# Optimization experiments

Hardware: AMD Instinct MI355X
Metric: run time of the kernel (lower is better)

The kernel has to match this reference:

```python
import jax, jax.numpy as jnp
import numpy as np

N = 100000
E = 1600000
IN_C = 128
OUT_C = 64
HID = 2 * OUT_C  # 128


def setup_inputs() -> dict:
    key = jax.random.key(0)
    ks = jax.random.split(key, 10)
    s = lambda fan_in: 1.0 / np.sqrt(fan_in)
    inp = {
        "x": jax.random.normal(ks[0], (N, IN_C), dtype=jnp.float32),
        "edge_index": jax.random.randint(ks[1], (2, E), 0, N, dtype=jnp.int64),
        # SAGEConv params: lin_l acts on aggregated neighbors (with bias), lin_r on root (no bias)
        "W1l": jax.random.uniform(ks[2], (IN_C, HID), jnp.float32, -s(IN_C), s(IN_C)),
        "b1": jnp.zeros((HID,), jnp.float32),
        "W1r": jax.random.uniform(ks[3], (IN_C, HID), jnp.float32, -s(IN_C), s(IN_C)),
        "Wml": jax.random.uniform(ks[4], (HID, OUT_C), jnp.float32, -s(HID), s(HID)),
        "bm": jnp.zeros((OUT_C,), jnp.float32),
        "Wmr": jax.random.uniform(ks[5], (HID, OUT_C), jnp.float32, -s(HID), s(HID)),
        "Wsl": jax.random.uniform(ks[6], (HID, OUT_C), jnp.float32, -s(HID), s(HID)),
        "bs": jnp.zeros((OUT_C,), jnp.float32),
        "Wsr": jax.random.uniform(ks[7], (HID, OUT_C), jnp.float32, -s(HID), s(HID)),
    }
    return inp


def _sage_mean(x, src, dst, Wl, b, Wr):
    n = x.shape[0]
    # mean aggregation of source features onto destination nodes
    agg = jax.ops.segment_sum(x[src], dst, num_segments=n)
    cnt = jax.ops.segment_sum(jnp.ones((src.shape[0],), x.dtype), dst, num_segments=n)
    agg = agg / jnp.maximum(cnt, 1.0)[:, None]
    return agg @ Wl + b + x @ Wr


def reference(x, edge_index, W1l, b1, W1r, Wml, bm, Wmr, Wsl, bs, Wsr):
    src, dst = edge_index[0], edge_index[1]
    h = jax.nn.relu(_sage_mean(x, src, dst, W1l, b1, W1r))
    mu = _sage_mean(h, src, dst, Wml, bm, Wmr)
    logstd = _sage_mean(h, src, dst, Wsl, bs, Wsr)
    return mu, logstd
```

## Files before the change

### kernel.cpp

```cpp
#include <hip/hip_runtime.h>


typedef __attribute__((ext_vector_type(8))) short bf16x8;
typedef __attribute__((ext_vector_type(4))) float f32x4;
typedef __attribute__((ext_vector_type(2))) float f32x2;

#define SHIFT 9
#define BW 512

__device__ __forceinline__ unsigned short f2bf(float f) {
    unsigned u = __builtin_bit_cast(unsigned, f);
    u += 0x7fff + ((u >> 16) & 1);
    return (unsigned short)(u >> 16);
}
__device__ __forceinline__ float bflo(unsigned u) { return __builtin_bit_cast(float, u << 16); }
__device__ __forceinline__ float bfh(unsigned u) { return __builtin_bit_cast(float, u); }

__global__ __launch_bounds__(256) void stage1_kernel(
    const float* __restrict__ x, const int* __restrict__ raw,
    const float* __restrict__ W1l, const float* __restrict__ W1r,
    const float* __restrict__ Wml, const float* __restrict__ Wmr,
    const float* __restrict__ Wsl, const float* __restrict__ Wsr,
    const float* __restrict__ bm, const float* __restrict__ bs,
    unsigned short* __restrict__ B1p, unsigned short* __restrict__ B2p,
    float* __restrict__ bc, unsigned short* __restrict__ A1,
    unsigned short* __restrict__ A2, int* __restrict__ bcnt,
    unsigned* __restrict__ recs, int n, int nE, int cap, int nBinA, int nXB) {
    const int b = blockIdx.x;
    const int t = threadIdx.x;
    if (b < nBinA) {
        __shared__ int cnt[256];
        __shared__ int cur[256];
        __shared__ int gbase[256];
        __shared__ int sflag;
        const int e0 = b * 4096;
        const int e1 = (e0 + 4096 < nE) ? e0 + 4096 : nE;
        int acc = 0;
        for (int e = e0 + t; e < e1; e += 256) acc |= raw[2 * e + 1];
        if (t == 0) sflag = 0;
        cnt[t] = 0;
        cur[t] = 0;
        __syncthreads();
        if (acc) atomicOr(&sflag, 1);
        __syncthreads();
        const bool is64 = (sflag == 0);
        for (int e = e0 + t; e < e1; e += 256) {
            int d = is64 ? raw[2 * (nE + e)] : raw[nE + e];
            atomicAdd(&cnt[d >> SHIFT], 1);
        }
        __syncthreads();
        gbase[t] = cnt[t] ? atomicAdd(&bcnt[t], cnt[t]) : 0;
        __syncthreads();
        for (int e = e0 + t; e < e1; e += 256) {
            int s, d;
            if (is64) { s = raw[2 * e]; d = raw[2 * (nE + e)]; }
            else      { s = raw[e];     d = raw[nE + e]; }
            int bk = d >> SHIFT;
            int pos = gbase[bk] + atomicAdd(&cur[bk], 1);
            if (pos < cap)
                recs[(size_t)bk * cap + pos] = ((unsigned)s << SHIFT) | (unsigned)(d & (BW - 1));
        }
    } else if (b < nBinA + nXB) {
        int i = ((b - nBinA) * 256 + t) * 4;
        if (i < n * 128) {
            float4 v = *reinterpret_cast<const float4*>(x + i);
            int row = i >> 7, col = i & 127;
            unsigned short* p = A1 + (size_t)row * 256 + 128 + col;
            p[0] = f2bf(v.x); p[1] = f2bf(v.y); p[2] = f2bf(v.z); p[3] = f2bf(v.w);
        }
    } else if (b < nBinA + nXB + 128) {
        int i = (b - nBinA - nXB) * 256 + t;
        int j = i & 7, lq = (i >> 3) & 63, ks = (i >> 9) & 7, nf = i >> 12;
        int k = ks * 32 + (lq >> 4) * 8 + j;
        int c = nf * 16 + (lq & 15);
        float w1 = (k < 128) ? W1l[k * 128 + c] : W1r[(k - 128) * 128 + c];
        float w2;
        if (k < 128) w2 = (c < 64) ? Wml[k * 64 + c] : Wsl[k * 64 + (c - 64)];
        else         w2 = (c < 64) ? Wmr[(k - 128) * 64 + c] : Wsr[(k - 128) * 64 + (c - 64)];
        B1p[i] = f2bf(w1);
        B2p[i] = f2bf(w2);
        if (i < 128) bc[i] = (i < 64) ? bm[i] : bs[i - 64];
    } else {
        if (t < 64) {
            ((unsigned*)A1)[(size_t)n * 128 + 64 + t] = 0;
            ((unsigned*)A2)[(size_t)n * 128 + 64 + t] = 0;
        }
    }
}

__global__ __launch_bounds__(256) void binB_kernel(
    const unsigned* __restrict__ recs, const int* __restrict__ bcnt,
    int* __restrict__ rowptrP, int* __restrict__ cnts,
    int* __restrict__ csr, int cap, int n, int NB) {
    __shared__ int sdeg[BW];
    __shared__ int scur[BW];
    __shared__ int ssum[256];
    const int b = blockIdx.x;
    const int t = threadIdx.x;
    const int node0 = b << SHIFT;

    int rawb = (t < NB) ? bcnt[t] : 0;
    ssum[t] = rawb;
    __syncthreads();
    for (int off = 1; off < 256; off <<= 1) {
        int val = (t >= off) ? ssum[t - off] : 0;
        __syncthreads();
        ssum[t] += val;
        __syncthreads();
    }
    const int base = ((b == 0) ? 0 : ssum[b - 1]) + b * 3 * BW;
    int cnt = bcnt[b];
    if (cnt > cap) cnt = cap;
    const unsigned* r = recs + (size_t)b * cap;
    __syncthreads();

    sdeg[t] = 0;
    sdeg[t + 256] = 0;
    __syncthreads();
    for (int i = t; i < cnt; i += 256) atomicAdd(&sdeg[r[i] & (BW - 1)], 1);
    __syncthreads();
    int d0 = sdeg[2 * t], d1 = sdeg[2 * t + 1];
    int p0 = (d0 + 3) & ~3, p1 = (d1 + 3) & ~3;
    int sum = p0 + p1;
    ssum[t] = sum;
    __syncthreads();
    for (int off = 1; off < 256; off <<= 1) {
        int val = (t >= off) ? ssum[t - off] : 0;
        __syncthreads();
        ssum[t] += val;
        __syncthreads();
    }
    int ex = ssum[t] - sum;
    scur[2 * t] = ex;
    scur[2 * t + 1] = ex + p0;
    __syncthreads();
#pragma unroll
    for (int q = 0; q < 2; ++q) {
        int i = 2 * t + q;
        int node = node0 + i;
        if (node < n) {
            rowptrP[node] = base + scur[i];
            cnts[node] = sdeg[i];
        }
    }
    __syncthreads();
    for (int i = t; i < cnt; i += 256) {
        unsigned rec = r[i];
        int pos = base + atomicAdd(&scur[rec & (BW - 1)], 1);
        csr[pos] = (int)(rec >> SHIFT);
    }
    __syncthreads();
#pragma unroll
    for (int q = 0; q < 2; ++q) {
        int i = 2 * t + q;
        int node = node0 + i;
        if (node < n) {
            int d = sdeg[i];
            int pad = (4 - (d & 3)) & 3;
            int st = base + scur[i];
            for (int k = 0; k < pad; ++k) csr[st + k] = n;
        }
    }
}

__global__ __launch_bounds__(256) void gather_kernel(const unsigned int* __restrict__ feat,
                                                     const int* __restrict__ rowptrP,
                                                     const int* __restrict__ cnts,
                                                     const int* __restrict__ csr,
                                                     unsigned int* __restrict__ agg, int n) {
    int wv = (blockIdx.x * 256 + threadIdx.x) >> 6;
    if (wv >= n) return;
    int lane = threadIdx.x & 63;
    int eg = lane >> 4;
    int c4 = (lane & 15) * 4;
    int beg = rowptrP[wv];
    int deg = cnts[wv];
    int endp = beg + ((deg + 3) & ~3);
    f32x2 a0 = (f32x2)(0.f), a1 = (f32x2)(0.f), a2 = (f32x2)(0.f), a3 = (f32x2)(0.f);
    int jb = beg;
    if (jb < endp) {
        int s = csr[jb + eg];
        uint4 v = *reinterpret_cast<const uint4*>(feat + (size_t)s * 128 + c4);
#pragma unroll 2
        for (jb += 4; jb < endp; jb += 4) {
            int s2 = csr[jb + eg];
            uint4 v2 = *reinterpret_cast<const uint4*>(feat + (size_t)s2 * 128 + c4);
            a0 += (f32x2){bflo(v.x), bfh(v.x)};
            a1 += (f32x2){bflo(v.y), bfh(v.y)};
            a2 += (f32x2){bflo(v.z), bfh(v.z)};
            a3 += (f32x2){bflo(v.w), bfh(v.w)};
            v = v2;
        }
        a0 += (f32x2){bflo(v.x), bfh(v.x)};
        a1 += (f32x2){bflo(v.y), bfh(v.y)};
        a2 += (f32x2){bflo(v.z), bfh(v.z)};
        a3 += (f32x2){bflo(v.w), bfh(v.w)};
    }
    float acc[8] = {a0.x, a0.y, a1.x, a1.y, a2.x, a2.y, a3.x, a3.y};
#pragma unroll
    for (int q = 0; q < 8; ++q) {
        acc[q] += __shfl_xor(acc[q], 16);
        acc[q] += __shfl_xor(acc[q], 32);
    }
    if (eg == 0) {
        float ic = 1.0f / fmaxf((float)deg, 1.0f);
        uint4 r;
        r.x = (unsigned)f2bf(acc[0] * ic) | ((unsigned)f2bf(acc[1] * ic) << 16);
        r.y = (unsigned)f2bf(acc[2] * ic) | ((unsigned)f2bf(acc[3] * ic) << 16);
        r.z = (unsigned)f2bf(acc[4] * ic) | ((unsigned)f2bf(acc[5] * ic) << 16);
        r.w = (unsigned)f2bf(acc[6] * ic) | ((unsigned)f2bf(acc[7] * ic) << 16);
        *reinterpret_cast<uint4*>(agg + (size_t)wv * 128 + c4) = r;
    }
}

template <int MODE>
__global__ __launch_bounds__(256) void mfma_gemm(const unsigned short* __restrict__ A,
                                                 const unsigned short* __restrict__ Bp,
                                                 const float* __restrict__ bias,
                                                 void* __restrict__ outp, int n) {
    const int tid = threadIdx.x;
    const int w = tid >> 6, l = tid & 63;
    const int lr = l & 15;
    const int lg = l >> 4;
    const int row0 = blockIdx.x * 128 + w * 32;

    f32x4 acc[2][8];
#pragma unroll
    for (int mf = 0; mf < 2; ++mf)
#pragma unroll
        for (int nf = 0; nf < 8; ++nf) acc[mf][nf] = (f32x4)(0.0f);

    int r0 = row0 + lr;       if (r0 > n - 1) r0 = n - 1;
    int r1 = row0 + 16 + lr;  if (r1 > n - 1) r1 = n - 1;
    const unsigned short* a0p = A + (size_t)r0 * 256 + lg * 8;
    const unsigned short* a1p = A + (size_t)r1 * 256 + lg * 8;
    const unsigned short* bp = Bp + (size_t)l * 8;

    for (int ks = 0; ks < 8; ++ks) {
        bf16x8 a0 = *reinterpret_cast<const bf16x8*>(a0p + ks * 32);
        bf16x8 a1 = *reinterpret_cast<const bf16x8*>(a1p + ks * 32);
#pragma unroll
        for (int nf = 0; nf < 8; ++nf) {
            bf16x8 b = *reinterpret_cast<const bf16x8*>(bp + ((nf * 8 + ks) << 9));
            acc[0][nf] = __builtin_amdgcn_mfma_f32_16x16x32_bf16(a0, b, acc[0][nf], 0, 0, 0);
            acc[1][nf] = __builtin_amdgcn_mfma_f32_16x16x32_bf16(a1, b, acc[1][nf], 0, 0, 0);
        }
    }

    float bv[8];
#pragma unroll
    for (int nf = 0; nf < 8; ++nf) bv[nf] = bias[nf * 16 + lr];

#pragma unroll
    for (int mf = 0; mf < 2; ++mf)
#pragma unroll
        for (int j = 0; j < 4; ++j) {
            int row = row0 + mf * 16 + lg * 4 + j;
            if (row >= n) continue;
#pragma unroll
            for (int nf = 0; nf < 8; ++nf) {
                int col = nf * 16 + lr;
                float v = acc[mf][nf][j] + bv[nf];
                if (MODE == 0) {
                    v = fmaxf(v, 0.0f);
                    ((unsigned short*)outp)[(size_t)row * 256 + 128 + col] = f2bf(v);
                } else {
                    float* o = (float*)outp;
                    if (col < 64) o[(size_t)row * 64 + col] = v;
                    else o[(size_t)n * 64 + (size_t)row * 64 + (col - 64)] = v;
                }
            }
        }
}

extern "C" void kernel_launch(void* const* d_in, const int* in_sizes, int n_in,
                              void* d_out, int out_size, void* d_ws, size_t ws_size,
                              hipStream_t stream) {
    const float* x = (const float*)d_in[0];
    const int* eidx_raw = (const int*)d_in[1];
    const float* W1l = (const float*)d_in[2];
    const float* b1 = (const float*)d_in[3];
    const float* W1r = (const float*)d_in[4];
    const float* Wml = (const float*)d_in[5];
    const float* bm = (const float*)d_in[6];
    const float* Wmr = (const float*)d_in[7];
    const float* Wsl = (const float*)d_in[8];
    const float* bs = (const float*)d_in[9];
    const float* Wsr = (const float*)d_in[10];
    float* out = (float*)d_out;

    const int n = in_sizes[0] / 128;
    const int nE = in_sizes[1] / 2;

    const int NB = ((n - 1) >> SHIFT) + 1;
    long long capll = (((long long)nE << SHIFT) / n) * 5 / 4 + 1024;
    const int cap = (int)((capll + 15) & ~15LL);
    const int csr_ints = nE + NB * 3 * BW + 64;

    char* ws = (char*)d_ws;
    const size_t a_bytes = (size_t)(n + 1) * 512;
    const size_t a1_off = 0;
    const size_t a2_off = a1_off + a_bytes;
    const size_t recs_off = a2_off;
    const size_t csr_off = a2_off + a_bytes;
    const size_t rowptr_off = csr_off + (size_t)csr_ints * 4;
    const size_t cnts_off = rowptr_off + (size_t)n * 4;
    const size_t bcnt_off = cnts_off + (size_t)n * 4;
    const size_t b1p_off = (bcnt_off + 1024 + 255) & ~(size_t)255;
    const size_t b2p_off = b1p_off + 65536;
    const size_t bc_off = b2p_off + 65536;

    unsigned short* A1 = (unsigned short*)(ws + a1_off);
    unsigned short* A2 = (unsigned short*)(ws + a2_off);
    unsigned* recs = (unsigned*)(ws + recs_off);
    int* csr = (int*)(ws + csr_off);
    int* rowptrP = (int*)(ws + rowptr_off);
    int* cnts = (int*)(ws + cnts_off);
    int* bcnt = (int*)(ws + bcnt_off);
    unsigned short* B1p = (unsigned short*)(ws + b1p_off);
    unsigned short* B2p = (unsigned short*)(ws + b2p_off);
    float* bc = (float*)(ws + bc_off);

    hipMemsetAsync(bcnt, 0, 1024, stream);

    const int nBinA = (nE + 4095) / 4096;
    const int nXB = (n * 32 + 255) / 256;
    stage1_kernel<<<nBinA + nXB + 129, 256, 0, stream>>>(
        x, eidx_raw, W1l, W1r, Wml, Wmr, Wsl, Wsr, bm, bs,
        B1p, B2p, bc, A1, A2, bcnt, recs, n, nE, cap, nBinA, nXB);

    binB_kernel<<<NB, 256, 0, stream>>>(recs, bcnt, rowptrP, cnts, csr, cap, n, NB);

    const int gather_blocks = (n * 64 + 255) / 256;
    const int gemm_blocks = (n + 127) / 128;

    gather_kernel<<<gather_blocks, 256, 0, stream>>>(
        (const unsigned int*)A1 + 64, rowptrP, cnts, csr, (unsigned int*)A1, n);
    mfma_gemm<0><<<gemm_blocks, 256, 0, stream>>>(A1, B1p, b1, A2, n);

    gather_kernel<<<gather_blocks, 256, 0, stream>>>(
        (const unsigned int*)A2 + 64, rowptrP, cnts, csr, (unsigned int*)A2, n);
    mfma_gemm<1><<<gemm_blocks, 256, 0, stream>>>(A2, B2p, bc, out, n);
}
```

Measured before the change: 264.4 us.

## Halve bucket width and fuse x conversion into CSR build kernel

Bucket width drops to 256 nodes so the CSR-building pass launches about twice as many blocks. The x-to-bf16 conversion and weight packing move out of the edge-binning kernel and are co-scheduled with the CSR build. The x conversion now processes 8 floats per thread with a single 16-byte store. The aim is better device occupancy in the latency-bound binning stage and overlap with bandwidth-bound conversion. In exchange, binning uses more shared counters and does more global atomics per block.

```diff
diff --git a/kernel.cpp b/kernel.cpp
--- a/kernel.cpp
+++ b/kernel.cpp
@@ -5,8 +5,9 @@
 typedef __attribute__((ext_vector_type(4))) float f32x4;
 typedef __attribute__((ext_vector_type(2))) float f32x2;
 
-#define SHIFT 9
-#define BW 512
+#define SHIFT 8
+#define BW 256
+#define NBMAX 512
 
 __device__ __forceinline__ unsigned short f2bf(float f) {
     unsigned u = __builtin_bit_cast(unsigned, f);
@@ -16,60 +17,131 @@
 __device__ __forceinline__ float bflo(unsigned u) { return __builtin_bit_cast(float, u << 16); }
 __device__ __forceinline__ float bfh(unsigned u) { return __builtin_bit_cast(float, u); }
 
-__global__ __launch_bounds__(256) void stage1_kernel(
-    const float* __restrict__ x, const int* __restrict__ raw,
+__global__ __launch_bounds__(256) void binA_kernel(
+    const int* __restrict__ raw, int* __restrict__ bcnt,
+    unsigned* __restrict__ recs, int nE, int cap) {
+    __shared__ int cnt[NBMAX];
+    __shared__ int cur[NBMAX];
+    __shared__ int gbase[NBMAX];
+    __shared__ int sflag;
+    const int t = threadIdx.x;
+    const int e0 = blockIdx.x * 2048;
+    const int e1 = (e0 + 2048 < nE) ? e0 + 2048 : nE;
+    int acc = 0;
+    for (int e = e0 + t; e < e1; e += 256) acc |= raw[2 * e + 1];
+    if (t == 0) sflag = 0;
+    cnt[t] = 0; cnt[t + 256] = 0;
+    cur[t] = 0; cur[t + 256] = 0;
+    __syncthreads();
+    if (acc) atomicOr(&sflag, 1);
+    __syncthreads();
+    const bool is64 = (sflag == 0);
+    for (int e = e0 + t; e < e1; e += 256) {
+        int d = is64 ? raw[2 * (nE + e)] : raw[nE + e];
+        atomicAdd(&cnt[d >> SHIFT], 1);
+    }
+    __syncthreads();
+    gbase[t] = cnt[t] ? atomicAdd(&bcnt[t], cnt[t]) : 0;
+    gbase[t + 256] = cnt[t + 256] ? atomicAdd(&bcnt[t + 256], cnt[t + 256]) : 0;
+    __syncthreads();
+    for (int e = e0 + t; e < e1; e += 256) {
+        int s, d;
+        if (is64) { s = raw[2 * e]; d = raw[2 * (nE + e)]; }
+        else      { s = raw[e];     d = raw[nE + e]; }
+        int bk = d >> SHIFT;
+        int pos = gbase[bk] + atomicAdd(&cur[bk], 1);
+        if (pos < cap)
+            recs[(size_t)bk * cap + pos] = ((unsigned)s << SHIFT) | (unsigned)(d & (BW - 1));
+    }
+}
+
+__global__ __launch_bounds__(256) void k2_kernel(
+    const unsigned* __restrict__ recs, const int* __restrict__ bcnt,
+    int* __restrict__ rowptrP, int* __restrict__ cnts, int* __restrict__ csr,
+    const float* __restrict__ x,
     const float* __restrict__ W1l, const float* __restrict__ W1r,
     const float* __restrict__ Wml, const float* __restrict__ Wmr,
     const float* __restrict__ Wsl, const float* __restrict__ Wsr,
     const float* __restrict__ bm, const float* __restrict__ bs,
     unsigned short* __restrict__ B1p, unsigned short* __restrict__ B2p,
     float* __restrict__ bc, unsigned short* __restrict__ A1,
-    unsigned short* __restrict__ A2, int* __restrict__ bcnt,
-    unsigned* __restrict__ recs, int n, int nE, int cap, int nBinA, int nXB) {
+    unsigned short* __restrict__ A2,
+    int cap, int n, int nE, int NB, int nXB) {
+    __shared__ int sdeg[BW];
+    __shared__ int scur[BW];
+    __shared__ int sscan[256];
+    __shared__ int sb[NBMAX];
     const int b = blockIdx.x;
     const int t = threadIdx.x;
-    if (b < nBinA) {
-        __shared__ int cnt[256];
-        __shared__ int cur[256];
-        __shared__ int gbase[256];
-        __shared__ int sflag;
-        const int e0 = b * 4096;
-        const int e1 = (e0 + 4096 < nE) ? e0 + 4096 : nE;
-        int acc = 0;
-        for (int e = e0 + t; e < e1; e += 256) acc |= raw[2 * e + 1];
-        if (t == 0) sflag = 0;
-        cnt[t] = 0;
-        cur[t] = 0;
-        __syncthreads();
-        if (acc) atomicOr(&sflag, 1);
-        __syncthreads();
-        const bool is64 = (sflag == 0);
-        for (int e = e0 + t; e < e1; e += 256) {
-            int d = is64 ? raw[2 * (nE + e)] : raw[nE + e];
-            atomicAdd(&cnt[d >> SHIFT], 1);
-        }
-        __syncthreads();
-        gbase[t] = cnt[t] ? atomicAdd(&bcnt[t], cnt[t]) : 0;
-        __syncthreads();
-        for (int e = e0 + t; e < e1; e += 256) {
-            int s, d;
-            if (is64) { s = raw[2 * e]; d = raw[2 * (nE + e)]; }
-            else      { s = raw[e];     d = raw[nE + e]; }
-            int bk = d >> SHIFT;
-            int pos = gbase[bk] + atomicAdd(&cur[bk], 1);
-            if (pos < cap)
-                recs[(size_t)bk * cap + pos] = ((unsigned)s << SHIFT) | (unsigned)(d & (BW - 1));
-        }
-    } else if (b < nBinA + nXB) {
-        int i = ((b - nBinA) * 256 + t) * 4;
+    if (b < NB) {
+        int v0 = (2 * t < NB) ? bcnt[2 * t] : 0;
+        int v1 = (2 * t + 1 < NB) ? bcnt[2 * t + 1] : 0;
+        int sum = v0 + v1;
+        sscan[t] = sum;
+        __syncthreads();
+        for (int off = 1; off < 256; off <<= 1) {
+            int val = (t >= off) ? sscan[t - off] : 0;
+            __syncthreads();
+            sscan[t] += val;
+            __syncthreads();
+        }
+        int ex = sscan[t] - sum;
+        sb[2 * t] = ex;
+        sb[2 * t + 1] = ex + v0;
+        __syncthreads();
+        const int base = sb[b] + b * 3 * BW;
+        int cnt = bcnt[b];
+        if (cnt > cap) cnt = cap;
+        const unsigned* r = recs + (size_t)b * cap;
+
+        sdeg[t] = 0;
+        __syncthreads();
+        for (int i = t; i < cnt; i += 256) atomicAdd(&sdeg[r[i] & (BW - 1)], 1);
+        __syncthreads();
+        int d = sdeg[t];
+        int p = (d + 3) & ~3;
+        sscan[t] = p;
+        __syncthreads();
+        for (int off = 1; off < 256; off <<= 1) {
+            int val = (t >= off) ? sscan[t - off] : 0;
+            __syncthreads();
+            sscan[t] += val;
+            __syncthreads();
+        }
+        int exn = sscan[t] - p;
+        scur[t] = exn;
+        const int node = (b << SHIFT) + t;
+        if (node < n) {
+            rowptrP[node] = base + exn;
+            cnts[node] = d;
+        }
+        __syncthreads();
+        for (int i = t; i < cnt; i += 256) {
+            unsigned rec = r[i];
+            int pos = base + atomicAdd(&scur[rec & (BW - 1)], 1);
+            csr[pos] = (int)(rec >> SHIFT);
+        }
+        __syncthreads();
+        if (node < n) {
+            int pad = (4 - (d & 3)) & 3;
+            int st = base + scur[t];
+            for (int k = 0; k < pad; ++k) csr[st + k] = n;
+        }
+    } else if (b < NB + nXB) {
+        int i = ((b - NB) * 256 + t) * 8;
         if (i < n * 128) {
-            float4 v = *reinterpret_cast<const float4*>(x + i);
+            float4 va = *reinterpret_cast<const float4*>(x + i);
+            float4 vb = *reinterpret_cast<const float4*>(x + i + 4);
             int row = i >> 7, col = i & 127;
-            unsigned short* p = A1 + (size_t)row * 256 + 128 + col;
-            p[0] = f2bf(v.x); p[1] = f2bf(v.y); p[2] = f2bf(v.z); p[3] = f2bf(v.w);
-        }
-    } else if (b < nBinA + nXB + 128) {
-        int i = (b - nBinA - nXB) * 256 + t;
+            uint4 r;
+            r.x = (unsigned)f2bf(va.x) | ((unsigned)f2bf(va.y) << 16);
+            r.y = (unsigned)f2bf(va.z) | ((unsigned)f2bf(va.w) << 16);
+            r.z = (unsigned)f2bf(vb.x) | ((unsigned)f2bf(vb.y) << 16);
+            r.w = (unsigned)f2bf(vb.z) | ((unsigned)f2bf(vb.w) << 16);
+            *reinterpret_cast<uint4*>(A1 + (size_t)row * 256 + 128 + col) = r;
+        }
+    } else if (b < NB + nXB + 128) {
+        int i = (b - NB - nXB) * 256 + t;
         int j = i & 7, lq = (i >> 3) & 63, ks = (i >> 9) & 7, nf = i >> 12;
         int k = ks * 32 + (lq >> 4) * 8 + j;
         int c = nf * 16 + (lq & 15);
@@ -84,81 +156,6 @@
         if (t < 64) {
             ((unsigned*)A1)[(size_t)n * 128 + 64 + t] = 0;
             ((unsigned*)A2)[(size_t)n * 128 + 64 + t] = 0;
-        }
-    }
-}
-
-__global__ __launch_bounds__(256) void binB_kernel(
-    const unsigned* __restrict__ recs, const int* __restrict__ bcnt,
-    int* __restrict__ rowptrP, int* __restrict__ cnts,
-    int* __restrict__ csr, int cap, int n, int NB) {
-    __shared__ int sdeg[BW];
-    __shared__ int scur[BW];
-    __shared__ int ssum[256];
-    const int b = blockIdx.x;
-    const int t = threadIdx.x;
-    const int node0 = b << SHIFT;
-
-    int rawb = (t < NB) ? bcnt[t] : 0;
-    ssum[t] = rawb;
-    __syncthreads();
-    for (int off = 1; off < 256; off <<= 1) {
-        int val = (t >= off) ? ssum[t - off] : 0;
-        __syncthreads();
-        ssum[t] += val;
-        __syncthreads();
-    }
-    const int base = ((b == 0) ? 0 : ssum[b - 1]) + b * 3 * BW;
-    int cnt = bcnt[b];
-    if (cnt > cap) cnt = cap;
-    const unsigned* r = recs + (size_t)b * cap;
-    __syncthreads();
-
-    sdeg[t] = 0;
-    sdeg[t + 256] = 0;
-    __syncthreads();
-    for (int i = t; i < cnt; i += 256) atomicAdd(&sdeg[r[i] & (BW - 1)], 1);
-    __syncthreads();
-    int d0 = sdeg[2 * t], d1 = sdeg[2 * t + 1];
-    int p0 = (d0 + 3) & ~3, p1 = (d1 + 3) & ~3;
-    int sum = p0 + p1;
-    ssum[t] = sum;
-    __syncthreads();
-    for (int off = 1; off < 256; off <<= 1) {
-        int val = (t >= off) ? ssum[t - off] : 0;
-        __syncthreads();
-        ssum[t] += val;
-        __syncthreads();
-    }
-    int ex = ssum[t] - sum;
-    scur[2 * t] = ex;
-    scur[2 * t + 1] = ex + p0;
-    __syncthreads();
-#pragma unroll
-    for (int q = 0; q < 2; ++q) {
-        int i = 2 * t + q;
-        int node = node0 + i;
-        if (node < n) {
-            rowptrP[node] = base + scur[i];
-            cnts[node] = sdeg[i];
-        }
-    }
-    __syncthreads();
-    for (int i = t; i < cnt; i += 256) {
-        unsigned rec = r[i];
-        int pos = base + atomicAdd(&scur[rec & (BW - 1)], 1);
-        csr[pos] = (int)(rec >> SHIFT);
-    }
-    __syncthreads();
-#pragma unroll
-    for (int q = 0; q < 2; ++q) {
-        int i = 2 * t + q;
-        int node = node0 + i;
-        if (node < n) {
-            int d = sdeg[i];
-            int pad = (4 - (d & 3)) & 3;
-            int st = base + scur[i];
-            for (int k = 0; k < pad; ++k) csr[st + k] = n;
         }
     }
 }
@@ -306,7 +303,7 @@
     const size_t rowptr_off = csr_off + (size_t)csr_ints * 4;
     const size_t cnts_off = rowptr_off + (size_t)n * 4;
     const size_t bcnt_off = cnts_off + (size_t)n * 4;
-    const size_t b1p_off = (bcnt_off + 1024 + 255) & ~(size_t)255;
+    const size_t b1p_off = (bcnt_off + 2048 + 255) & ~(size_t)255;
     const size_t b2p_off = b1p_off + 65536;
     const size_t bc_off = b2p_off + 65536;
 
@@ -321,15 +318,14 @@
     unsigned short* B2p = (unsigned short*)(ws + b2p_off);
     float* bc = (float*)(ws + bc_off);
 
-    hipMemsetAsync(bcnt, 0, 1024, stream);
-
-    const int nBinA = (nE + 4095) / 4096;
-    const int nXB = (n * 32 + 255) / 256;
-    stage1_kernel<<<nBinA + nXB + 129, 256, 0, stream>>>(
-        x, eidx_raw, W1l, W1r, Wml, Wmr, Wsl, Wsr, bm, bs,
-        B1p, B2p, bc, A1, A2, bcnt, recs, n, nE, cap, nBinA, nXB);
-
-    binB_kernel<<<NB, 256, 0, stream>>>(recs, bcnt, rowptrP, cnts, csr, cap, n, NB);
+    hipMemsetAsync(bcnt, 0, 2048, stream);
+
+    binA_kernel<<<(nE + 2047) / 2048, 256, 0, stream>>>(eidx_raw, bcnt, recs, nE, cap);
+
+    const int nXB = (n * 128 / 8 + 255) / 256;
+    k2_kernel<<<NB + nXB + 129, 256, 0, stream>>>(
+        recs, bcnt, rowptrP, cnts, csr, x, W1l, W1r, Wml, Wmr, Wsl, Wsr,
+        bm, bs, B1p, B2p, bc, A1, A2, cap, n, nE, NB, nXB);
 
     const int gather_blocks = (n * 64 + 255) / 256;
     const int gemm_blocks = (n + 127) / 128;
```

New measurement: 262.5 us, median of 2. Within noise of the previous version (-0.8%).
